# Optimization experiments

Hardware: AMD Instinct MI355X
Metric: run time of the kernel (lower is better)

## Reference

```python
import jax, jax.numpy as jnp
import numpy as np

THRESH = 0.5
MARGIN = 0.1
SCALE_POS = 2.0
SCALE_NEG = 40.0
EPS = 1e-5


def setup_inputs() -> dict:
    key = jax.random.key(0)
    k1, k2 = jax.random.split(key)
    B, D, NUM_CLASSES = 4096, 512, 512
    feats = jax.random.normal(k1, (B, D), dtype=jnp.float32)
    feats = feats / jnp.linalg.norm(feats, axis=1, keepdims=True)  # unit-norm embeddings
    labels = jax.random.randint(k2, (B,), 0, NUM_CLASSES, dtype=jnp.int64)
    return {"feats": feats, "labels": labels, "label_num": 26}


def reference(feats, labels, label_num):
    B = feats.shape[0]
    sim = feats @ feats.T  # [B, B]
    same = labels[:, None] == labels[None, :]
    pos_m = same & (sim < 1.0 - EPS)      # pos_pair_ mask per row
    neg_m = ~same                         # neg_pair_ mask per row
    has_pos = pos_m.any(axis=1)
    has_neg = neg_m.any(axis=1)
    min_pos = jnp.min(jnp.where(pos_m, sim, jnp.inf), axis=1)
    max_neg = jnp.max(jnp.where(neg_m, sim, -jnp.inf), axis=1)
    pos_thr = jnp.where(has_pos, min_pos, jnp.float32(0.2))  # fallback when no pos pairs
    neg_thr = jnp.where(has_neg, max_neg, jnp.float32(0.8))  # fallback when no neg pairs
    # mined pairs (same semantics as the per-row boolean filtering)
    neg_pair = neg_m & (sim + MARGIN > pos_thr[:, None])
    pos_pair = pos_m & (sim - MARGIN < neg_thr[:, None])
    valid = pos_pair.any(axis=1) & neg_pair.any(axis=1) & (jnp.arange(B) < B - label_num)
    # masked log-sum-exp style reductions (exp of -inf on masked entries -> 0)
    pos_sum = jnp.sum(jnp.exp(jnp.where(pos_pair, -SCALE_POS * (sim - THRESH), -jnp.inf)), axis=1)
    neg_sum = jnp.sum(jnp.exp(jnp.where(neg_pair, SCALE_NEG * (sim - THRESH), -jnp.inf)), axis=1)
    per_row = (1.0 / SCALE_POS) * jnp.log1p(pos_sum) + (1.0 / SCALE_NEG) * jnp.log1p(neg_sum)
    return jnp.sum(jnp.where(valid, per_row, 0.0)) / B
```

## Files before the change

### kernel.cpp

```cpp
#include <hip/hip_runtime.h>
#include <stdint.h>

#define BN 4096
#define DK 512
#define THRESH 0.5f
#define MARGIN 0.1f

typedef __attribute__((ext_vector_type(4))) float f32x4;
typedef __attribute__((ext_vector_type(8))) unsigned short ushort8;

__device__ __forceinline__ unsigned short f2bf(float f) {
    unsigned u = __float_as_uint(f);
    u += 0x7FFFu + ((u >> 16) & 1u);
    return (unsigned short)(u >> 16);
}
__device__ __forceinline__ float bf2f(unsigned short b) {
    return __uint_as_float((unsigned)b << 16);
}

__device__ __forceinline__ unsigned char f2fp8(float x) {
    float a = fabsf(x);
    unsigned s = (__float_as_uint(x) >> 24) & 0x80u;
    if (a >= 448.f) return (unsigned char)(s | 0x7E);
    if (a < 0.015625f) {
        int m = (int)(a * 512.0f + 0.5f);
        return (unsigned char)(s | m);
    }
    unsigned u = __float_as_uint(a);
    u += 0x0FFFFFu + ((u >> 20) & 1u);
    unsigned e = (u >> 23) - 127u + 7u;
    unsigned m = (u >> 20) & 7u;
    if (e >= 16u) return (unsigned char)(s | 0x7E);
    return (unsigned char)(s | (e << 3) | m);
}

__device__ __forceinline__ void async_cp16(void* lds, const void* g) {
    __builtin_amdgcn_global_load_lds(
        (const __attribute__((address_space(1))) void*)g,
        (__attribute__((address_space(3))) void*)lds,
        16, 0, 0);
}

__global__ void cvt_kernel(const float4* __restrict__ in, uchar4* __restrict__ out,
                           float* __restrict__ loss_out) {
    int i = blockIdx.x * blockDim.x + threadIdx.x;
    float4 v = in[i];
    uchar4 o;
    o.x = f2fp8(v.x); o.y = f2fp8(v.y); o.z = f2fp8(v.z); o.w = f2fp8(v.w);
    out[i] = o;
    if (blockIdx.x == 0 && threadIdx.x == 0) loss_out[0] = 0.f;
}

__global__ __launch_bounds__(256, 4) void ms_gemm(
    const unsigned char* __restrict__ Fb,
    unsigned short* __restrict__ simb)
{
    __shared__ __align__(16) unsigned char SMEMB[32768];
    unsigned char* As = SMEMB;
    unsigned char* Bs = SMEMB + 16384;
    unsigned short* SMEM = (unsigned short*)SMEMB;

    const int t    = threadIdx.x;
    const int lane = t & 63;
    const int w    = t >> 6;
    const int wr   = w >> 1, wc = w & 1;
    const int quad = lane >> 4;
    const int cIdx = lane & 15;

    int l = blockIdx.x, by = 0;
    while (l >= 32 - by) { l -= (32 - by); ++by; }
    const int bx = by + l;
    const int rowBase = by * 128;
    const int colBase = bx * 128;
    const bool diag = (by == bx);
    const unsigned char* Bsel = diag ? As : Bs;

    f32x4 acc[4][4];
#pragma unroll
    for (int i = 0; i < 4; ++i)
#pragma unroll
        for (int j = 0; j < 4; ++j) acc[i][j] = (f32x4){0.f, 0.f, 0.f, 0.f};

    for (int k0 = 0; k0 < DK; k0 += 128) {
#pragma unroll
        for (int it = 0; it < 4; ++it) {
            const int id = it * 256 + t;
            const int r  = id >> 3;
            const int gc = (id & 7) ^ (r & 7);
            async_cp16(As + id * 16,
                       Fb + (size_t)(rowBase + r) * DK + k0 + gc * 16);
        }
        if (!diag) {
#pragma unroll
            for (int it = 0; it < 4; ++it) {
                const int id = it * 256 + t;
                const int r  = id >> 3;
                const int gc = (id & 7) ^ (r & 7);
                async_cp16(Bs + id * 16,
                           Fb + (size_t)(colBase + r) * DK + k0 + gc * 16);
            }
        }
        __syncthreads();

#pragma unroll
        for (int kk = 0; kk < 4; ++kk) {
            long af[4], bg[4];
#pragma unroll
            for (int im = 0; im < 4; ++im) {
                int r = wr * 64 + im * 16 + cIdx;
                int u = kk * 4 + quad;
                int p = (u >> 1) ^ (r & 7);
                af[im] = *reinterpret_cast<const long*>(
                    &As[r * 128 + p * 16 + (u & 1) * 8]);
            }
#pragma unroll
            for (int jn = 0; jn < 4; ++jn) {
                int c = wc * 64 + jn * 16 + cIdx;
                int u = kk * 4 + quad;
                int p = (u >> 1) ^ (c & 7);
                bg[jn] = *reinterpret_cast<const long*>(
                    &Bsel[c * 128 + p * 16 + (u & 1) * 8]);
            }
#pragma unroll
            for (int im = 0; im < 4; ++im)
#pragma unroll
                for (int jn = 0; jn < 4; ++jn)
                    acc[im][jn] = __builtin_amdgcn_mfma_f32_16x16x32_fp8_fp8(
                        af[im], bg[jn], acc[im][jn], 0, 0, 0);
        }
        __syncthreads();
    }

#pragma unroll
    for (int im = 0; im < 4; ++im)
#pragma unroll
        for (int rg = 0; rg < 4; ++rg) {
            const int grow = rowBase + wr * 64 + im * 16 + quad * 4 + rg;
            unsigned short* dst = simb + (size_t)grow * BN + colBase + wc * 64 + cIdx;
#pragma unroll
            for (int jn = 0; jn < 4; ++jn)
                dst[jn * 16] = f2bf(acc[im][jn][rg]);
        }

    if (diag) return;

#pragma unroll
    for (int im = 0; im < 4; ++im)
#pragma unroll
        for (int jn = 0; jn < 4; ++jn) {
            ushort4 v;
            v.x = f2bf(acc[im][jn][0]);
            v.y = f2bf(acc[im][jn][1]);
            v.z = f2bf(acc[im][jn][2]);
            v.w = f2bf(acc[im][jn][3]);
            const int c  = wc * 64 + jn * 16 + cIdx;
            const int r  = wr * 64 + im * 16 + quad * 4;
            const int r8 = r >> 3;
            const int ri = r & 7;
            *reinterpret_cast<ushort4*>(
                &SMEM[c * 128 + ((r8 ^ (c & 15)) << 3) + ri]) = v;
        }
    __syncthreads();

    const int lch = t & 7;
    const int trw = t >> 3;
#pragma unroll
    for (int it = 0; it < 4; ++it) {
        const int tr = it * 32 + trw;
        const int q1 = lch ^ (tr & 15);
        const int q2 = (lch + 8) ^ (tr & 15);
        ushort8 a = *reinterpret_cast<const ushort8*>(&SMEM[tr * 128 + q1 * 8]);
        ushort8 b = *reinterpret_cast<const ushort8*>(&SMEM[tr * 128 + q2 * 8]);
        unsigned short* dst = simb + (size_t)(colBase + tr) * BN + rowBase;
        *reinterpret_cast<ushort8*>(&dst[lch * 8])       = a;
        *reinterpret_cast<ushort8*>(&dst[(lch + 8) * 8]) = b;
    }
}

__global__ __launch_bounds__(256) void ms_rows(
    const unsigned short* __restrict__ simb,
    const int* __restrict__ labels,
    const int* __restrict__ label_num,
    float* __restrict__ out)
{
    __shared__ int   labT[8][512];
    __shared__ float bsum[4];

    const int t    = threadIdx.x;
    const int lane = t & 63;
    const int w    = t >> 6;

    for (int i = t; i < BN; i += 256) labT[i & 7][i >> 3] = labels[i];
    __syncthreads();

    const int lim = BN - label_num[0];
    const int row = blockIdx.x * 4 + w;
    const int lr  = labT[row & 7][row >> 3];
    const ushort8* rp = (const ushort8*)(simb + (size_t)row * BN);

    ushort8 d[8];
    uint64_t mpos = 0, msame = 0;
    float mn = INFINITY, mx = -INFINITY;
#pragma unroll
    for (int j = 0; j < 8; ++j) {
        d[j] = rp[j * 64 + lane];
        const int c8 = j * 64 + lane;
#pragma unroll
        for (int e = 0; e < 8; ++e) {
            const int col = c8 * 8 + e;
            const float s = bf2f(d[j][e]);
            const bool same = (labT[e][c8] == lr);
            const bool pos  = same && (col != row);
            if (pos)   mn = fminf(mn, s);
            if (!same) mx = fmaxf(mx, s);
            msame |= (uint64_t)same << (j * 8 + e);
            mpos  |= (uint64_t)pos  << (j * 8 + e);
        }
    }
#pragma unroll
    for (int off = 1; off < 64; off <<= 1) {
        mn = fminf(mn, __shfl_xor(mn, off, 64));
        mx = fmaxf(mx, __shfl_xor(mx, off, 64));
    }
    const float tP = (mn < 1e30f)  ? mn : 0.2f;
    const float tN = (mx > -1e30f) ? mx : 0.8f;

    float ps = 0.f, ns = 0.f;
    bool anyN = false;
#pragma unroll
    for (int j = 0; j < 8; ++j)
#pragma unroll
        for (int e = 0; e < 8; ++e) {
            const int k = j * 8 + e;
            const float s = bf2f(d[j][e]);
            const bool doP = ((mpos >> k) & 1) && (s - MARGIN < tN);
            if (__any(doP))
                ps += doP ? __expf(-2.0f * (s - THRESH)) : 0.f;
            const bool doN = !((msame >> k) & 1) && (s + MARGIN > tP);
            anyN |= doN;
            const bool doNe = doN && (s > 0.125f);
            if (__any(doNe))
                ns += doNe ? __expf(40.0f * (s - THRESH)) : 0.f;
        }
#pragma unroll
    for (int off = 1; off < 64; off <<= 1) {
        ps += __shfl_xor(ps, off, 64);
        ns += __shfl_xor(ns, off, 64);
    }
    const bool anyNw = __any(anyN);
    float wsum = 0.f;
    if (lane == 0 && ps > 0.f && anyNw && row < lim)
        wsum = 0.5f * log1pf(ps) + 0.025f * log1pf(ns);

    if (lane == 0) bsum[w] = wsum;
    __syncthreads();
    if (t == 0)
        atomicAdd(out, (bsum[0] + bsum[1] + bsum[2] + bsum[3]) * (1.0f / (float)BN));
}

extern "C" void kernel_launch(void* const* d_in, const int* in_sizes, int n_in,
                              void* d_out, int out_size, void* d_ws, size_t ws_size,
                              hipStream_t stream)
{
    const float* feats     = (const float*)d_in[0];
    const int*   labels    = (const int*)d_in[1];
    const int*   label_num = (const int*)d_in[2];
    float*       out       = (float*)d_out;

    char* ws = (char*)d_ws;
    unsigned char*  Fb   = (unsigned char*)ws;
    unsigned short* simb = (unsigned short*)(ws + 4u * 1024u * 1024u);

    cvt_kernel<<<2048, 256, 0, stream>>>((const float4*)feats, (uchar4*)Fb, out);

    ms_gemm<<<528, 256, 0, stream>>>(Fb, simb);

    ms_rows<<<1024, 256, 0, stream>>>(simb, labels, label_num, out);
}
```

Baseline: 109.8 us.

## Double-buffer LDS tiles in fp8 similarity GEMM to overlap loads with MFMA

Enlarges the GEMM's shared-memory staging to two 32KB buffers. The next K-slice's async global-to-LDS copies are now issued before the MFMAs run on the current slice, which also removes one barrier per K step. The intent is to hide global load latency behind compute. In exchange, LDS use per block doubles and launch bounds drop to 2 blocks per CU, so fewer waves are resident. An extra barrier is added before the epilogue reuses shared memory.

```diff
diff --git a/kernel.cpp b/kernel.cpp
--- a/kernel.cpp
+++ b/kernel.cpp
@@ -51,13 +51,11 @@
     if (blockIdx.x == 0 && threadIdx.x == 0) loss_out[0] = 0.f;
 }
 
-__global__ __launch_bounds__(256, 4) void ms_gemm(
+__global__ __launch_bounds__(256, 2) void ms_gemm(
     const unsigned char* __restrict__ Fb,
     unsigned short* __restrict__ simb)
 {
-    __shared__ __align__(16) unsigned char SMEMB[32768];
-    unsigned char* As = SMEMB;
-    unsigned char* Bs = SMEMB + 16384;
+    __shared__ __align__(16) unsigned char SMEMB[65536];
     unsigned short* SMEM = (unsigned short*)SMEMB;
 
     const int t    = threadIdx.x;
@@ -73,7 +71,6 @@
     const int rowBase = by * 128;
     const int colBase = bx * 128;
     const bool diag = (by == bx);
-    const unsigned char* Bsel = diag ? As : Bs;
 
     f32x4 acc[4][4];
 #pragma unroll
@@ -81,26 +78,55 @@
 #pragma unroll
         for (int j = 0; j < 4; ++j) acc[i][j] = (f32x4){0.f, 0.f, 0.f, 0.f};
 
-    for (int k0 = 0; k0 < DK; k0 += 128) {
+    const int id0 = t;
+#pragma unroll
+    for (int it = 0; it < 4; ++it) {
+        const int id = it * 256 + id0;
+        const int r  = id >> 3;
+        const int gc = (id & 7) ^ (r & 7);
+        async_cp16(SMEMB + id * 16,
+                   Fb + (size_t)(rowBase + r) * DK + 0 + gc * 16);
+    }
+    if (!diag) {
 #pragma unroll
         for (int it = 0; it < 4; ++it) {
-            const int id = it * 256 + t;
+            const int id = it * 256 + id0;
             const int r  = id >> 3;
             const int gc = (id & 7) ^ (r & 7);
-            async_cp16(As + id * 16,
-                       Fb + (size_t)(rowBase + r) * DK + k0 + gc * 16);
-        }
-        if (!diag) {
+            async_cp16(SMEMB + 16384 + id * 16,
+                       Fb + (size_t)(colBase + r) * DK + 0 + gc * 16);
+        }
+    }
+
+#pragma unroll
+    for (int s = 0; s < 4; ++s) {
+        __syncthreads();
+
+        if (s < 3) {
+            const int k1 = (s + 1) * 128;
+            unsigned char* dstA = SMEMB + ((s + 1) & 1) * 32768;
 #pragma unroll
             for (int it = 0; it < 4; ++it) {
-                const int id = it * 256 + t;
+                const int id = it * 256 + id0;
                 const int r  = id >> 3;
                 const int gc = (id & 7) ^ (r & 7);
-                async_cp16(Bs + id * 16,
-                           Fb + (size_t)(colBase + r) * DK + k0 + gc * 16);
+                async_cp16(dstA + id * 16,
+                           Fb + (size_t)(rowBase + r) * DK + k1 + gc * 16);
             }
-        }
-        __syncthreads();
+            if (!diag) {
+#pragma unroll
+                for (int it = 0; it < 4; ++it) {
+                    const int id = it * 256 + id0;
+                    const int r  = id >> 3;
+                    const int gc = (id & 7) ^ (r & 7);
+                    async_cp16(dstA + 16384 + id * 16,
+                               Fb + (size_t)(colBase + r) * DK + k1 + gc * 16);
+                }
+            }
+        }
+
+        const unsigned char* As   = SMEMB + (s & 1) * 32768;
+        const unsigned char* Bsel = diag ? As : (As + 16384);
 
 #pragma unroll
         for (int kk = 0; kk < 4; ++kk) {
@@ -128,7 +154,6 @@
                     acc[im][jn] = __builtin_amdgcn_mfma_f32_16x16x32_fp8_fp8(
                         af[im], bg[jn], acc[im][jn], 0, 0, 0);
         }
-        __syncthreads();
     }
 
 #pragma unroll
@@ -143,6 +168,8 @@
         }
 
     if (diag) return;
+
+    __syncthreads();
 
 #pragma unroll
     for (int im = 0; im < 4; ++im)
```

Result: no change. 110.5 us (+0.7%).
